# Optimization experiments

Hardware: AMD Instinct MI355X
Metric: run time of the kernel (lower is better)

## Reference

```python
import jax, jax.numpy as jnp
import numpy as np

TOKEN_SIZE = 4
NEIGHBOR_SIZE = 3


def setup_inputs() -> dict:
    key = jax.random.key(0)
    ks = jax.random.split(key, 8)
    B, C, H, W = 8, 256, 64, 64
    return {
        "blue_feat": jax.random.normal(ks[0], (B, C, H, W), jnp.float32),
        "white_feat": jax.random.normal(ks[1], (B, C, H, W), jnp.float32),
        "Wq": jax.random.normal(ks[2], (C, C), jnp.float32) * 0.05,
        "bq": jax.random.normal(ks[3], (C,), jnp.float32) * 0.05,
        "Wk": jax.random.normal(ks[4], (C, C), jnp.float32) * 0.05,
        "bk": jax.random.normal(ks[5], (C,), jnp.float32) * 0.05,
        "Wv": jax.random.normal(ks[6], (C, C), jnp.float32) * 0.05,
        "bv": jax.random.normal(ks[7], (C,), jnp.float32) * 0.05,
    }


def _tokens(x, nh, nw, ts):
    # [B,C,H,W] -> [B,nh,nw,C,ts*ts]
    B, C = x.shape[0], x.shape[1]
    return (x.reshape(B, C, nh, ts, nw, ts)
             .transpose(0, 2, 4, 1, 3, 5)
             .reshape(B, nh, nw, C, ts * ts))


def reference(blue_feat, white_feat, Wq, bq, Wk, bk, Wv, bv):
    ts, ns = TOKEN_SIZE, NEIGHBOR_SIZE
    pad = ns // 2
    B, C, H, W = blue_feat.shape
    scale = float((ts * ts) ** -0.5)

    # 1x1 conv projections (pointwise channel mix + bias)
    Q = jnp.einsum('bchw,oc->bohw', blue_feat, Wq) + bq[None, :, None, None]
    K = jnp.einsum('bchw,oc->bohw', white_feat, Wk) + bk[None, :, None, None]
    V = jnp.einsum('bchw,oc->bohw', white_feat, Wv) + bv[None, :, None, None]

    nh, nw = H // ts, W // ts  # H,W divisible by ts -> no padding branch
    Qt = _tokens(Q, nh, nw, ts)  # [B,nh,nw,C,D]
    Kt = _tokens(K, nh, nw, ts)
    Vt = _tokens(V, nh, nw, ts)

    # zero-padded token grid, gather 3x3 neighbor tokens (F.unfold equivalent)
    padw = ((0, 0), (pad, pad), (pad, pad), (0, 0), (0, 0))
    Kp = jnp.pad(Kt, padw)
    Vp = jnp.pad(Vt, padw)
    Knb = jnp.stack([Kp[:, di:di + nh, dj:dj + nw]
                     for di in range(ns) for dj in range(ns)], axis=3)  # [B,nh,nw,9,C,D]
    Vnb = jnp.stack([Vp[:, di:di + nh, dj:dj + nw]
                     for di in range(ns) for dj in range(ns)], axis=3)

    # per-channel attention over neighbor tokens
    attn = jax.nn.softmax(
        jnp.einsum('bhwcd,bhwncd->bhwcn', Qt, Knb) * scale, axis=-1)
    out = jnp.einsum('bhwcn,bhwncd->bhwcd', attn, Vnb)  # [B,nh,nw,C,D]

    enhanced = (out.reshape(B, nh, nw, C, ts, ts)
                   .transpose(0, 3, 1, 4, 2, 5)
                   .reshape(B, C, H, W))
    return blue_feat + enhanced  # out_proj is Identity since c1 == c2
```

## Files before the change

kernel.cpp:

```cpp
#include <hip/hip_runtime.h>
#include <hip/hip_bf16.h>
#include <stdint.h>

typedef float  f32x4  __attribute__((ext_vector_type(4)));
typedef float  f32x2  __attribute__((ext_vector_type(2)));
typedef __bf16 bf16x8 __attribute__((ext_vector_type(8)));

#define LROW 40

__global__ __launch_bounds__(256) void wprep_kernel(
    const float* __restrict__ Wq, const float* __restrict__ Wk,
    const float* __restrict__ Wv, __bf16* __restrict__ Wbf)
{
  const int b = blockIdx.x;
  const int t = b >> 5;
  const float* src = (t == 0) ? Wq : (t == 1) ? Wk : Wv;
  const int off = (b & 31) * 2048 + threadIdx.x * 8;
  f32x4 v0 = *(const f32x4*)(src + off);
  f32x4 v1 = *(const f32x4*)(src + off + 4);
  bf16x8 r;
#pragma unroll
  for (int q = 0; q < 4; ++q) { r[q] = (__bf16)v0[q]; r[q + 4] = (__bf16)v1[q]; }
  *(bf16x8*)(Wbf + t * 65536 + off) = r;
}


__global__ __launch_bounds__(256) void proj_gemm2_kernel(
    const float* __restrict__ blue, const float* __restrict__ white,
    const __bf16* __restrict__ Wbf,
    const float* __restrict__ bq, const float* __restrict__ bk,
    const float* __restrict__ bv,
    __bf16* __restrict__ Qt, __bf16* __restrict__ Kt, __bf16* __restrict__ Vt)
{
  __shared__ __bf16 Bs[2][128 * LROW];

  const int bidhw = blockIdx.x;
  const int lid   = (bidhw & 7) * 96 + (bidhw >> 3);
  const int nb    = lid / 3;
  const int ty    = lid - nb * 3;

  const float* X = (ty == 0) ? blue : white;
  const __bf16 *W0, *W1; const float *bias0, *bias1;
  __bf16 *Out0, *Out1; int oo0, oo1;
  if (ty == 0)      { W0 = Wbf;                     W1 = Wbf + 128 * 256;
                      bias0 = bq; bias1 = bq; Out0 = Qt; Out1 = Qt; oo0 = 0;   oo1 = 128; }
  else if (ty == 1) { W0 = Wbf + 65536;             W1 = Wbf + 2 * 65536;
                      bias0 = bk; bias1 = bv; Out0 = Kt; Out1 = Vt; oo0 = 0;   oo1 = 0;   }
  else              { W0 = Wbf + 65536 + 128 * 256; W1 = Wbf + 2 * 65536 + 128 * 256;
                      bias0 = bk; bias1 = bv; Out0 = Kt; Out1 = Vt; oo0 = 128; oo1 = 128; }

  const int tid  = threadIdx.x;
  const int lane = tid & 63;
  const int wave = tid >> 6;
  const int wo   = wave >> 1;
  const int wn   = wave & 1;

  const int n0    = nb * 128;
  const int batch = n0 >> 12;
  const int p0    = n0 & 4095;
  const int tk0   = p0 >> 4;
  const int trow  = tk0 >> 4;
  const int tcol0 = tk0 & 15;
  const float* Xb = X + (size_t)batch * (256 * 4096);

  const int n2   = tid & 63;
  const int ko   = tid >> 6;
  const int nloc = 2 * n2;
  const int tl   = nloc >> 4;
  const int d    = nloc & 15;
  const int hw   = (trow * 4 + (d >> 2)) * 64 + (tcol0 + tl) * 4 + (d & 3);
  const float* srcB0 = Xb + (size_t)(ko * 8) * 4096 + hw;

  f32x2 pre[8];
#define LOADB(kk) { const float* s_ = srcB0 + (size_t)(kk) * 32 * 4096;            \
    pre[0] = *(const f32x2*)(s_);         pre[1] = *(const f32x2*)(s_ + 4096);     \
    pre[2] = *(const f32x2*)(s_ + 8192);  pre[3] = *(const f32x2*)(s_ + 12288);    \
    pre[4] = *(const f32x2*)(s_ + 16384); pre[5] = *(const f32x2*)(s_ + 20480);    \
    pre[6] = *(const f32x2*)(s_ + 24576); pre[7] = *(const f32x2*)(s_ + 28672); }

  const int lrow = lane & 15;
  const int lk   = (lane >> 4) * 8;
  const int aoff = (wo * 64 + lrow) * 256 + lk;

  f32x4 acc[2][4][4];
#pragma unroll
  for (int p = 0; p < 2; ++p)
#pragma unroll
    for (int i = 0; i < 4; ++i)
#pragma unroll
      for (int j = 0; j < 4; ++j) acc[p][i][j] = (f32x4)0.0f;

  LOADB(0);

  for (int kk = 0; kk < 8; ++kk) {
    __bf16* bsw = &Bs[kk & 1][0];
    bf16x8 r0, r1;
#pragma unroll
    for (int t = 0; t < 8; ++t) { r0[t] = (__bf16)pre[t][0]; r1[t] = (__bf16)pre[t][1]; }
    *(bf16x8*)(bsw + (nloc + 0) * LROW + ko * 8) = r0;
    *(bf16x8*)(bsw + (nloc + 1) * LROW + ko * 8) = r1;

    bf16x8 af0[4], af1[4];
#pragma unroll
    for (int i = 0; i < 4; ++i) af0[i] = *(const bf16x8*)(W0 + aoff + i * 4096 + kk * 32);
#pragma unroll
    for (int i = 0; i < 4; ++i) af1[i] = *(const bf16x8*)(W1 + aoff + i * 4096 + kk * 32);

    if (kk < 7) LOADB(kk + 1);

    asm volatile("s_waitcnt lgkmcnt(0)" ::: "memory");
    __builtin_amdgcn_s_barrier();
    asm volatile("" ::: "memory");

    const __bf16* bsr = &Bs[kk & 1][0];
    bf16x8 bfrag[4];
#pragma unroll
    for (int j = 0; j < 4; ++j)
      bfrag[j] = *(const bf16x8*)(bsr + (wn * 64 + j * 16 + lrow) * LROW + lk);
#pragma unroll
    for (int i = 0; i < 4; ++i)
#pragma unroll
      for (int j = 0; j < 4; ++j) {
        acc[0][i][j] = __builtin_amdgcn_mfma_f32_16x16x32_bf16(af0[i], bfrag[j], acc[0][i][j], 0, 0, 0);
        acc[1][i][j] = __builtin_amdgcn_mfma_f32_16x16x32_bf16(af1[i], bfrag[j], acc[1][i][j], 0, 0, 0);
      }
  }
#undef LOADB

#pragma unroll
  for (int p = 0; p < 2; ++p) {
    const __bf16* Wdummy = p ? W1 : W0; (void)Wdummy;
    __bf16* Out = p ? Out1 : Out0;
    const float* bias = p ? bias1 : bias0;
    const int oo = p ? oo1 : oo0;
#pragma unroll
    for (int i = 0; i < 4; ++i) {
      const int orow = wo * 64 + i * 16 + (lane >> 4) * 4;
#pragma unroll
      for (int j = 0; j < 4; ++j) {
        const int n  = n0 + wn * 64 + j * 16 + (lane & 15);
        const int bb = n >> 12;
        const int pp = n & 4095;
        const int tt = pp >> 4;
        const int tii = tt >> 4;
        const int tjj = tt & 15;
        const int dd  = pp & 15;
        const size_t base = ((size_t)(bb * 16 + tii) * 256) * 256 + tjj * 16 + dd;
#pragma unroll
        for (int r = 0; r < 4; ++r) {
          const int o = oo + orow + r;
          const float v = acc[p][i][j][r] + bias[o];
          Out[base + (size_t)o * 256] = (__bf16)v;
        }
      }
    }
  }
}

__global__ __launch_bounds__(256) void proj_gemm_kernel(
    const float* __restrict__ blue, const float* __restrict__ white,
    const float* __restrict__ Wq, const float* __restrict__ bq,
    const float* __restrict__ Wk, const float* __restrict__ bk,
    const float* __restrict__ Wv, const float* __restrict__ bv,
    __bf16* __restrict__ Qt, __bf16* __restrict__ Kt, __bf16* __restrict__ Vt)
{
  __shared__ __bf16 As[128 * LROW];
  __shared__ __bf16 Bs[128 * LROW];

  const int bidhw = blockIdx.x;
  const int lid   = (bidhw & 7) * 192 + (bidhw >> 3);
  const int nb    = lid / 6;
  const int bt    = lid % 6;
  const int tensor = (bt < 4) ? 1 + (bt & 1) : 0;
  const int ob     = (bt < 4) ? (bt >> 1) : (bt & 1);

  const float* X    = (tensor == 0) ? blue : white;
  const float* W    = (tensor == 0) ? Wq : (tensor == 1) ? Wk : Wv;
  const float* bias = (tensor == 0) ? bq : (tensor == 1) ? bk : bv;
  __bf16*      Out  = (tensor == 0) ? Qt : (tensor == 1) ? Kt : Vt;

  const int tid  = threadIdx.x;
  const int lane = tid & 63;
  const int wave = tid >> 6;
  const int wo   = wave >> 1;
  const int wn   = wave & 1;

  const int o0 = ob * 128;
  const int n0 = nb * 128;
  const int batch = n0 >> 12;
  const int p0    = n0 & 4095;
  const int tk0   = p0 >> 4;
  const int trow  = tk0 >> 4;
  const int tcol0 = tk0 & 15;
  const float* Xb = X + (size_t)batch * (256 * 4096);

  f32x4 acc[4][4];
#pragma unroll
  for (int i = 0; i < 4; ++i)
#pragma unroll
    for (int j = 0; j < 4; ++j) acc[i][j] = (f32x4)0.0f;

  const int arow  = tid >> 1;
  const int ahalf = tid & 1;
  const int n2   = tid & 63;
  const int ko   = tid >> 6;
  const int nloc = 2 * n2;
  const int tl   = nloc >> 4;
  const int d    = nloc & 15;
  const int hw   = (trow * 4 + (d >> 2)) * 64 + (tcol0 + tl) * 4 + (d & 3);

  const int lrow = lane & 15;
  const int lk   = (lane >> 4) * 8;

  for (int kk = 0; kk < 8; ++kk) {
    const int k0 = kk * 32;
    {
      const float* src = W + (size_t)(o0 + arow) * 256 + k0 + ahalf * 16;
      f32x4 t0 = *(const f32x4*)(src + 0);
      f32x4 t1 = *(const f32x4*)(src + 4);
      f32x4 t2 = *(const f32x4*)(src + 8);
      f32x4 t3 = *(const f32x4*)(src + 12);
      bf16x8 c0, c1;
#pragma unroll
      for (int q = 0; q < 4; ++q) { c0[q] = (__bf16)t0[q]; c0[q + 4] = (__bf16)t1[q]; }
#pragma unroll
      for (int q = 0; q < 4; ++q) { c1[q] = (__bf16)t2[q]; c1[q + 4] = (__bf16)t3[q]; }
      __bf16* dst = As + arow * LROW + ahalf * 16;
      *(bf16x8*)(dst + 0) = c0;
      *(bf16x8*)(dst + 8) = c1;
    }
    {
      const float* src = Xb + (size_t)(k0 + ko * 8) * 4096 + hw;
      f32x2 v0 = *(const f32x2*)(src + 0 * 4096);
      f32x2 v1 = *(const f32x2*)(src + 1 * 4096);
      f32x2 v2 = *(const f32x2*)(src + 2 * 4096);
      f32x2 v3 = *(const f32x2*)(src + 3 * 4096);
      f32x2 v4 = *(const f32x2*)(src + 4 * 4096);
      f32x2 v5 = *(const f32x2*)(src + 5 * 4096);
      f32x2 v6 = *(const f32x2*)(src + 6 * 4096);
      f32x2 v7 = *(const f32x2*)(src + 7 * 4096);
      bf16x8 r0, r1;
      r0[0] = (__bf16)v0[0]; r0[1] = (__bf16)v1[0]; r0[2] = (__bf16)v2[0]; r0[3] = (__bf16)v3[0];
      r0[4] = (__bf16)v4[0]; r0[5] = (__bf16)v5[0]; r0[6] = (__bf16)v6[0]; r0[7] = (__bf16)v7[0];
      r1[0] = (__bf16)v0[1]; r1[1] = (__bf16)v1[1]; r1[2] = (__bf16)v2[1]; r1[3] = (__bf16)v3[1];
      r1[4] = (__bf16)v4[1]; r1[5] = (__bf16)v5[1]; r1[6] = (__bf16)v6[1]; r1[7] = (__bf16)v7[1];
      *(bf16x8*)(Bs + (nloc + 0) * LROW + ko * 8) = r0;
      *(bf16x8*)(Bs + (nloc + 1) * LROW + ko * 8) = r1;
    }
    __syncthreads();

    bf16x8 a[4], b[4];
#pragma unroll
    for (int i = 0; i < 4; ++i)
      a[i] = *(const bf16x8*)(As + (wo * 64 + i * 16 + lrow) * LROW + lk);
#pragma unroll
    for (int j = 0; j < 4; ++j)
      b[j] = *(const bf16x8*)(Bs + (wn * 64 + j * 16 + lrow) * LROW + lk);
#pragma unroll
    for (int i = 0; i < 4; ++i)
#pragma unroll
      for (int j = 0; j < 4; ++j)
        acc[i][j] = __builtin_amdgcn_mfma_f32_16x16x32_bf16(a[i], b[j], acc[i][j], 0, 0, 0);
    __syncthreads();
  }

#pragma unroll
  for (int i = 0; i < 4; ++i) {
    const int obase = o0 + wo * 64 + i * 16 + (lane >> 4) * 4;
#pragma unroll
    for (int j = 0; j < 4; ++j) {
      const int n  = n0 + wn * 64 + j * 16 + (lane & 15);
      const int bb = n >> 12;
      const int p  = n & 4095;
      const int tt = p >> 4;
      const int tii = tt >> 4;
      const int tjj = tt & 15;
      const int dd  = p & 15;
      const size_t base = ((size_t)(bb * 16 + tii) * 256) * 256 + tjj * 16 + dd;
#pragma unroll
      for (int r = 0; r < 4; ++r) {
        const int o = obase + r;
        const float v = acc[i][j][r] + bias[o];
        Out[base + (size_t)o * 256] = (__bf16)v;
      }
    }
  }
}

__device__ __forceinline__ void unpack8(const uint4 v, float* f) {
  const uint32_t u0 = v.x, u1 = v.y, u2 = v.z, u3 = v.w;
  f[0] = __uint_as_float(u0 << 16); f[1] = __uint_as_float(u0 & 0xffff0000u);
  f[2] = __uint_as_float(u1 << 16); f[3] = __uint_as_float(u1 & 0xffff0000u);
  f[4] = __uint_as_float(u2 << 16); f[5] = __uint_as_float(u2 & 0xffff0000u);
  f[6] = __uint_as_float(u3 << 16); f[7] = __uint_as_float(u3 & 0xffff0000u);
}

__global__ __launch_bounds__(256) void attn_kernel(
    const __bf16* __restrict__ Qt, const __bf16* __restrict__ Kt,
    const __bf16* __restrict__ Vt, const float* __restrict__ blue,
    float* __restrict__ out)
{
  const int j   = blockIdx.x;
  const int bid = (j & 7) * 256 + (j >> 3);
  const int cg  = bid & 15;
  const int ti  = (bid >> 4) & 15;
  const int b   = bid >> 8;

  const int tid = threadIdx.x;
  const int tj  = tid & 15;
  const int cl  = tid >> 4;
  const int c   = cg * 16 + cl;

  float q[16];
  {
    const __bf16* p = Qt + ((((size_t)b * 16 + ti) * 256 + c) * 16 + tj) * 16;
    unpack8(*(const uint4*)p, q);
    unpack8(*(const uint4*)(p + 8), q + 8);
  }

  float s[9];
#pragma unroll
  for (int n = 0; n < 9; ++n) {
    const int yi = ti + n / 3 - 1;
    const int yj = tj + n % 3 - 1;
    float dot = 0.0f;
    if (yi >= 0 && yi < 16 && yj >= 0 && yj < 16) {
      const __bf16* p = Kt + ((((size_t)b * 16 + yi) * 256 + c) * 16 + yj) * 16;
      float kf[16];
      unpack8(*(const uint4*)p, kf);
      unpack8(*(const uint4*)(p + 8), kf + 8);
#pragma unroll
      for (int dd = 0; dd < 16; ++dd) dot = fmaf(q[dd], kf[dd], dot);
    }
    s[n] = dot * 0.25f;
  }

  float m = s[0];
#pragma unroll
  for (int n = 1; n < 9; ++n) m = fmaxf(m, s[n]);
  float w[9], denom = 0.0f;
#pragma unroll
  for (int n = 0; n < 9; ++n) { w[n] = __expf(s[n] - m); denom += w[n]; }
  const float inv = 1.0f / denom;

  float o16[16];
#pragma unroll
  for (int dd = 0; dd < 16; ++dd) o16[dd] = 0.0f;
#pragma unroll
  for (int n = 0; n < 9; ++n) {
    const int yi = ti + n / 3 - 1;
    const int yj = tj + n % 3 - 1;
    if (yi >= 0 && yi < 16 && yj >= 0 && yj < 16) {
      const __bf16* p = Vt + ((((size_t)b * 16 + yi) * 256 + c) * 16 + yj) * 16;
      float vf[16];
      unpack8(*(const uint4*)p, vf);
      unpack8(*(const uint4*)(p + 8), vf + 8);
#pragma unroll
      for (int dd = 0; dd < 16; ++dd) o16[dd] = fmaf(w[n], vf[dd], o16[dd]);
    }
  }

  const size_t pbase = ((size_t)b * 256 + c) * 4096 + (size_t)(ti * 4) * 64 + tj * 4;
#pragma unroll
  for (int r = 0; r < 4; ++r) {
    f32x4 bl = *(const f32x4*)(blue + pbase + r * 64);
    f32x4 ov;
#pragma unroll
    for (int j2 = 0; j2 < 4; ++j2) ov[j2] = bl[j2] + o16[r * 4 + j2] * inv;
    *(f32x4*)(out + pbase + r * 64) = ov;
  }
}

extern "C" void kernel_launch(void* const* d_in, const int* in_sizes, int n_in,
                              void* d_out, int out_size, void* d_ws, size_t ws_size,
                              hipStream_t stream) {
  const float* blue  = (const float*)d_in[0];
  const float* white = (const float*)d_in[1];
  const float* Wq = (const float*)d_in[2];
  const float* bq = (const float*)d_in[3];
  const float* Wk = (const float*)d_in[4];
  const float* bk = (const float*)d_in[5];
  const float* Wv = (const float*)d_in[6];
  const float* bv = (const float*)d_in[7];
  float* out = (float*)d_out;

  const size_t tsz = (size_t)8 * 256 * 256 * 16;
  __bf16* Qt = (__bf16*)d_ws;
  __bf16* Kt = Qt + tsz;
  __bf16* Vt = Kt + tsz;

  const size_t need = (3 * tsz + 3 * 65536) * sizeof(__bf16);
  if (ws_size >= need) {
    __bf16* Wbf = Vt + tsz;
    wprep_kernel<<<96, 256, 0, stream>>>(Wq, Wk, Wv, Wbf);
    proj_gemm2_kernel<<<768, 256, 0, stream>>>(blue, white, Wbf, bq, bk, bv, Qt, Kt, Vt);
  } else {
    proj_gemm_kernel<<<1536, 256, 0, stream>>>(blue, white, Wq, bq, Wk, bk, Wv, bv, Qt, Kt, Vt);
  }
  attn_kernel<<<2048, 256, 0, stream>>>(Qt, Kt, Vt, blue, out);
}
```

Before: 76.17 us.

## Split projection GEMM into single-output tiles with two-deep input prefetch

Each projection block now computes a single 128x128 output tile instead of two, so the grid doubles to 1536 blocks. Accumulator registers are halved and launch bounds request 3 blocks per SM for more occupancy. The input staging loads two k-steps ahead using alternating prefetch register sets. In exchange, each activation tile is read from global memory twice as often across the blocks that share it.

```diff
diff --git a/kernel.cpp b/kernel.cpp
--- a/kernel.cpp
+++ b/kernel.cpp
@@ -25,7 +25,7 @@
 }
 
 
-__global__ __launch_bounds__(256) void proj_gemm2_kernel(
+__global__ __launch_bounds__(256, 3) void proj_gemm3_kernel(
     const float* __restrict__ blue, const float* __restrict__ white,
     const __bf16* __restrict__ Wbf,
     const float* __restrict__ bq, const float* __restrict__ bk,
@@ -35,19 +35,16 @@
   __shared__ __bf16 Bs[2][128 * LROW];
 
   const int bidhw = blockIdx.x;
-  const int lid   = (bidhw & 7) * 96 + (bidhw >> 3);
-  const int nb    = lid / 3;
-  const int ty    = lid - nb * 3;
-
-  const float* X = (ty == 0) ? blue : white;
-  const __bf16 *W0, *W1; const float *bias0, *bias1;
-  __bf16 *Out0, *Out1; int oo0, oo1;
-  if (ty == 0)      { W0 = Wbf;                     W1 = Wbf + 128 * 256;
-                      bias0 = bq; bias1 = bq; Out0 = Qt; Out1 = Qt; oo0 = 0;   oo1 = 128; }
-  else if (ty == 1) { W0 = Wbf + 65536;             W1 = Wbf + 2 * 65536;
-                      bias0 = bk; bias1 = bv; Out0 = Kt; Out1 = Vt; oo0 = 0;   oo1 = 0;   }
-  else              { W0 = Wbf + 65536 + 128 * 256; W1 = Wbf + 2 * 65536 + 128 * 256;
-                      bias0 = bk; bias1 = bv; Out0 = Kt; Out1 = Vt; oo0 = 128; oo1 = 128; }
+  const int lid   = (bidhw & 7) * 192 + (bidhw >> 3);
+  const int nb    = lid / 6;
+  const int bt    = lid % 6;
+  const int tensor = (bt < 4) ? 1 + (bt & 1) : 0;
+  const int ob     = (bt < 4) ? (bt >> 1) : (bt & 1);
+
+  const float* X    = (tensor == 0) ? blue : white;
+  const float* bias = (tensor == 0) ? bq : (tensor == 1) ? bk : bv;
+  __bf16*      Out  = (tensor == 0) ? Qt : (tensor == 1) ? Kt : Vt;
+  const __bf16* Wp  = Wbf + tensor * 65536 + ob * (128 * 256);
 
   const int tid  = threadIdx.x;
   const int lane = tid & 63;
@@ -55,6 +52,7 @@
   const int wo   = wave >> 1;
   const int wn   = wave & 1;
 
+  const int o0    = ob * 128;
   const int n0    = nb * 128;
   const int batch = n0 >> 12;
   const int p0    = n0 & 4095;
@@ -71,87 +69,78 @@
   const int hw   = (trow * 4 + (d >> 2)) * 64 + (tcol0 + tl) * 4 + (d & 3);
   const float* srcB0 = Xb + (size_t)(ko * 8) * 4096 + hw;
 
-  f32x2 pre[8];
-#define LOADB(kk) { const float* s_ = srcB0 + (size_t)(kk) * 32 * 4096;            \
-    pre[0] = *(const f32x2*)(s_);         pre[1] = *(const f32x2*)(s_ + 4096);     \
-    pre[2] = *(const f32x2*)(s_ + 8192);  pre[3] = *(const f32x2*)(s_ + 12288);    \
-    pre[4] = *(const f32x2*)(s_ + 16384); pre[5] = *(const f32x2*)(s_ + 20480);    \
-    pre[6] = *(const f32x2*)(s_ + 24576); pre[7] = *(const f32x2*)(s_ + 28672); }
-
   const int lrow = lane & 15;
   const int lk   = (lane >> 4) * 8;
   const int aoff = (wo * 64 + lrow) * 256 + lk;
 
-  f32x4 acc[2][4][4];
-#pragma unroll
-  for (int p = 0; p < 2; ++p)
-#pragma unroll
-    for (int i = 0; i < 4; ++i)
-#pragma unroll
-      for (int j = 0; j < 4; ++j) acc[p][i][j] = (f32x4)0.0f;
-
-  LOADB(0);
-
-  for (int kk = 0; kk < 8; ++kk) {
-    __bf16* bsw = &Bs[kk & 1][0];
-    bf16x8 r0, r1;
-#pragma unroll
-    for (int t = 0; t < 8; ++t) { r0[t] = (__bf16)pre[t][0]; r1[t] = (__bf16)pre[t][1]; }
-    *(bf16x8*)(bsw + (nloc + 0) * LROW + ko * 8) = r0;
-    *(bf16x8*)(bsw + (nloc + 1) * LROW + ko * 8) = r1;
-
-    bf16x8 af0[4], af1[4];
-#pragma unroll
-    for (int i = 0; i < 4; ++i) af0[i] = *(const bf16x8*)(W0 + aoff + i * 4096 + kk * 32);
-#pragma unroll
-    for (int i = 0; i < 4; ++i) af1[i] = *(const bf16x8*)(W1 + aoff + i * 4096 + kk * 32);
-
-    if (kk < 7) LOADB(kk + 1);
-
-    asm volatile("s_waitcnt lgkmcnt(0)" ::: "memory");
-    __builtin_amdgcn_s_barrier();
-    asm volatile("" ::: "memory");
-
-    const __bf16* bsr = &Bs[kk & 1][0];
-    bf16x8 bfrag[4];
-#pragma unroll
-    for (int j = 0; j < 4; ++j)
-      bfrag[j] = *(const bf16x8*)(bsr + (wn * 64 + j * 16 + lrow) * LROW + lk);
-#pragma unroll
-    for (int i = 0; i < 4; ++i)
-#pragma unroll
-      for (int j = 0; j < 4; ++j) {
-        acc[0][i][j] = __builtin_amdgcn_mfma_f32_16x16x32_bf16(af0[i], bfrag[j], acc[0][i][j], 0, 0, 0);
-        acc[1][i][j] = __builtin_amdgcn_mfma_f32_16x16x32_bf16(af1[i], bfrag[j], acc[1][i][j], 0, 0, 0);
-      }
-  }
+  f32x4 acc[4][4];
+#pragma unroll
+  for (int i = 0; i < 4; ++i)
+#pragma unroll
+    for (int j = 0; j < 4; ++j) acc[i][j] = (f32x4)0.0f;
+
+  f32x2 preA[8], preB[8];
+
+#define LOADB(P, kk) { const float* s_ = srcB0 + (size_t)(kk) * 32 * 4096;          \
+    P[0] = *(const f32x2*)(s_);         P[1] = *(const f32x2*)(s_ + 4096);          \
+    P[2] = *(const f32x2*)(s_ + 8192);  P[3] = *(const f32x2*)(s_ + 12288);         \
+    P[4] = *(const f32x2*)(s_ + 16384); P[5] = *(const f32x2*)(s_ + 20480);         \
+    P[6] = *(const f32x2*)(s_ + 24576); P[7] = *(const f32x2*)(s_ + 28672); }
+
+#define STEP(P, kk, BUF) {                                                          \
+    bf16x8 r0, r1;                                                                  \
+    _Pragma("unroll")                                                               \
+    for (int t = 0; t < 8; ++t) { r0[t] = (__bf16)P[t][0]; r1[t] = (__bf16)P[t][1]; } \
+    *(bf16x8*)(&Bs[BUF][0] + (nloc + 0) * LROW + ko * 8) = r0;                      \
+    *(bf16x8*)(&Bs[BUF][0] + (nloc + 1) * LROW + ko * 8) = r1;                      \
+    bf16x8 af[4];                                                                   \
+    _Pragma("unroll")                                                               \
+    for (int i = 0; i < 4; ++i)                                                     \
+      af[i] = *(const bf16x8*)(Wp + aoff + i * 4096 + (kk) * 32);                   \
+    if ((kk) + 2 < 8) LOADB(P, (kk) + 2);                                           \
+    asm volatile("s_waitcnt lgkmcnt(0)" ::: "memory");                              \
+    __builtin_amdgcn_s_barrier();                                                   \
+    asm volatile("" ::: "memory");                                                  \
+    bf16x8 bfrag[4];                                                                \
+    _Pragma("unroll")                                                               \
+    for (int j = 0; j < 4; ++j)                                                     \
+      bfrag[j] = *(const bf16x8*)(&Bs[BUF][0] + (wn * 64 + j * 16 + lrow) * LROW + lk); \
+    _Pragma("unroll")                                                               \
+    for (int i = 0; i < 4; ++i)                                                     \
+      _Pragma("unroll")                                                             \
+      for (int j = 0; j < 4; ++j)                                                   \
+        acc[i][j] = __builtin_amdgcn_mfma_f32_16x16x32_bf16(af[i], bfrag[j], acc[i][j], 0, 0, 0); \
+  }
+
+  LOADB(preA, 0);
+  LOADB(preB, 1);
+
+#pragma unroll
+  for (int kp = 0; kp < 4; ++kp) {
+    STEP(preA, 2 * kp,     0);
+    STEP(preB, 2 * kp + 1, 1);
+  }
+#undef STEP
 #undef LOADB
 
 #pragma unroll
-  for (int p = 0; p < 2; ++p) {
-    const __bf16* Wdummy = p ? W1 : W0; (void)Wdummy;
-    __bf16* Out = p ? Out1 : Out0;
-    const float* bias = p ? bias1 : bias0;
-    const int oo = p ? oo1 : oo0;
-#pragma unroll
-    for (int i = 0; i < 4; ++i) {
-      const int orow = wo * 64 + i * 16 + (lane >> 4) * 4;
-#pragma unroll
-      for (int j = 0; j < 4; ++j) {
-        const int n  = n0 + wn * 64 + j * 16 + (lane & 15);
-        const int bb = n >> 12;
-        const int pp = n & 4095;
-        const int tt = pp >> 4;
-        const int tii = tt >> 4;
-        const int tjj = tt & 15;
-        const int dd  = pp & 15;
-        const size_t base = ((size_t)(bb * 16 + tii) * 256) * 256 + tjj * 16 + dd;
-#pragma unroll
-        for (int r = 0; r < 4; ++r) {
-          const int o = oo + orow + r;
-          const float v = acc[p][i][j][r] + bias[o];
-          Out[base + (size_t)o * 256] = (__bf16)v;
-        }
+  for (int i = 0; i < 4; ++i) {
+    const int obase = o0 + wo * 64 + i * 16 + (lane >> 4) * 4;
+#pragma unroll
+    for (int j = 0; j < 4; ++j) {
+      const int n  = n0 + wn * 64 + j * 16 + (lane & 15);
+      const int bb = n >> 12;
+      const int pp = n & 4095;
+      const int tt = pp >> 4;
+      const int tii = tt >> 4;
+      const int tjj = tt & 15;
+      const int dd  = pp & 15;
+      const size_t base = ((size_t)(bb * 16 + tii) * 256) * 256 + tjj * 16 + dd;
+#pragma unroll
+      for (int r = 0; r < 4; ++r) {
+        const int o = obase + r;
+        const float v = acc[i][j][r] + bias[o];
+        Out[base + (size_t)o * 256] = (__bf16)v;
       }
     }
   }
@@ -393,7 +382,7 @@
   if (ws_size >= need) {
     __bf16* Wbf = Vt + tsz;
     wprep_kernel<<<96, 256, 0, stream>>>(Wq, Wk, Wv, Wbf);
-    proj_gemm2_kernel<<<768, 256, 0, stream>>>(blue, white, Wbf, bq, bk, bv, Qt, Kt, Vt);
+    proj_gemm3_kernel<<<1536, 256, 0, stream>>>(blue, white, Wbf, bq, bk, bv, Qt, Kt, Vt);
   } else {
     proj_gemm_kernel<<<1536, 256, 0, stream>>>(blue, white, Wq, bq, Wk, bk, Wv, bv, Qt, Kt, Vt);
   }
```

Measured after the change: 81.85 us. 1.07x slower.
